# Performance work log

Hardware: AMD Instinct MI355X
Metric: run time of the kernel (lower is better)

The kernel has to match this reference:

```python
import jax, jax.numpy as jnp
import numpy as np

K_NEIGHBORS = 3
CLASSES = 5


def _l2_norm(x):
    # x: (N, C, H, W) -> (N, H*W, C), unit L2 norm over channel dim
    N, C, H, W = x.shape
    x = x.reshape(N, C, H * W).transpose(0, 2, 1)
    return x / jnp.linalg.norm(x, axis=-1, keepdims=True)


def setup_inputs() -> dict:
    key = jax.random.key(0)
    k1, k2 = jax.random.split(key)
    anchor = jax.random.normal(k1, (32, 64, 21, 21), dtype=jnp.float32)
    support_set = jax.random.normal(k2, (25, 64, 21, 21), dtype=jnp.float32)
    return {"anchor": anchor, "support_set": support_set, "av_num": 1, "sav_num": 1}


def reference(anchor, support_set, av_num, sav_num):
    # anchor: (B*AV, C, H, W), support_set: (L*S, C, H, W)
    q = _l2_norm(anchor)            # (B, HW, C)
    s = _l2_norm(support_set)       # (L*S, HW, C)
    C = s.shape[-1]
    s_flat = s.reshape(-1, C)       # (M, C), M = L*S*HW (class-major)
    # dense cosine similarity: (B, HW, M)
    sim = jnp.einsum('bqc,mc->bqm', q, s_flat)
    B, HW, M = sim.shape
    per_cls = M // CLASSES
    # (B//av, av, HW, L, S*HW)
    sim = sim.reshape(B // av_num, av_num, HW, CLASSES, per_cls)
    sim = jax.nn.sigmoid(sim)
    # av_num == 1 -> squeeze AV dim (matches torch squeeze(1) path)
    sim = sim[:, 0] if av_num == 1 else jnp.power(jnp.prod(sim, axis=1), 1.0 / av_num)
    # per-class top-k over descriptors, sum over k and over query locations
    topk = jax.lax.top_k(sim, K_NEIGHBORS)[0]        # (B, HW, L, K)
    i2c_sim = topk.sum(axis=-1).sum(axis=-2)         # (B, L)
    return i2c_sim
```

## Files before the change

### kernel.cpp

```cpp
#include <hip/hip_runtime.h>
#include <hip/hip_bf16.h>
#include <math.h>

#define CLASSES     5
#define C_DIM       64
#define HW          441
#define B_ANCH      32
#define NSUP        25
#define NROWS       (B_ANCH*HW)
#define MSUP        (NSUP*HW)
#define PER_CLS     (MSUP/CLASSES)
#define TILE_COLS   32
#define ROW_BYTES   (C_DIM*2)
#define TILE_BYTES  (TILE_COLS*ROW_BYTES)
#define PER_CLS_PAD 2304
#define NPAD        (PER_CLS_PAD - PER_CLS)
#define QUARTERS    4
#define TILES_PER_Q 18
#define ROWS_PER_BLK 128
#define NBLK_X      ((NROWS + ROWS_PER_BLK - 1) / ROWS_PER_BLK)

#define NEG_INF  (-1e30f)

typedef __bf16 bf16x8 __attribute__((ext_vector_type(8)));
typedef float  f32x4  __attribute__((ext_vector_type(4)));

#define TOP3_INS(v, t0, t1, t2) do {                              \
    float _v = (v);                                               \
    float _n0 = fmaxf(_v, (t0));                                  \
    float _n1 = __builtin_amdgcn_fmed3f(_v, (t0), (t1));          \
    float _n2 = __builtin_amdgcn_fmed3f(_v, (t1), (t2));          \
    (t0) = _n0; (t1) = _n1; (t2) = _n2; } while (0)

#define TRIPLE_MERGE(u0, u1, u2, v0, v1, v2) do {                 \
    float _A = fminf((u0), (v0));                                 \
    float _B = fmaxf((u1), (v1));                                 \
    float _E = fmaxf((u2), (v2));                                 \
    float _m0 = fmaxf((u0), (v0));                                \
    float _m1 = __builtin_amdgcn_fmed3f((u0), (v0), _B);          \
    float _m2 = __builtin_amdgcn_fmed3f(_A, _B, _E);              \
    (u0) = _m0; (u1) = _m1; (u2) = _m2; } while (0)

typedef __attribute__((address_space(1))) const void g_void;
typedef __attribute__((address_space(3))) void l_void;
__device__ __forceinline__ void gload_lds16(const void* g, void* l) {
    __builtin_amdgcn_global_load_lds((g_void*)g, (l_void*)l, 16, 0, 0);
}

#define MFMA16(A, B, C) __builtin_amdgcn_mfma_f32_16x16x32_bf16((A), (B), (C), 0, 0, 0)

__global__ __launch_bounds__(256) void norm_rows_kernel(
    const float* __restrict__ anchor, const float* __restrict__ support,
    __bf16* __restrict__ qb, __bf16* __restrict__ sb) {
    int r = blockIdx.x * 256 + threadIdx.x;
    const int total_main = MSUP + NROWS;
    if (r >= total_main) {
        int i = r - total_main;
        if (i < CLASSES * NPAD) {
            int cls = i / NPAD, ix = PER_CLS + i % NPAD;
            __bf16* op = sb + ((size_t)cls * PER_CLS_PAD + ix) * C_DIM;
            bf16x8 z = {};
            #pragma unroll
            for (int c0 = 0; c0 < C_DIM; c0 += 8) *(bf16x8*)(op + c0) = z;
        }
        return;
    }
    bool isSup = r < MSUP;
    int rc = isSup ? r : r - MSUP;
    const float* in = isSup ? support : anchor;
    int img = rc / HW, p = rc % HW;
    const float* base = in + (size_t)img * C_DIM * HW + p;
    float q[C_DIM];
    float ss = 0.f;
    #pragma unroll
    for (int c = 0; c < C_DIM; ++c) { q[c] = base[c * HW]; ss += q[c] * q[c]; }
    float sc = rsqrtf(ss);
    __bf16* op;
    if (isSup) {
        int cls = rc / PER_CLS, ix = rc - cls * PER_CLS;
        op = sb + ((size_t)cls * PER_CLS_PAD + ix) * C_DIM;
    } else {
        op = qb + (size_t)rc * C_DIM;
    }
    #pragma unroll
    for (int c0 = 0; c0 < C_DIM; c0 += 8) {
        bf16x8 v;
        #pragma unroll
        for (int j = 0; j < 8; ++j) v[j] = (__bf16)(q[c0 + j] * sc);
        *(bf16x8*)(op + c0) = v;
    }
}

template<int QNT, bool TAIL>
__device__ __forceinline__ void gemm_quarter(
    const char* stage_src,
    char* smem_base,
    const char* pB,
    int xoff0, int xoff1,
    int stage_dst_off,
    int lane, int lr,
    const bf16x8 a0[2], const bf16x8 a1[2],
    float t0[2][4], float t1[2][4], float t2[2][4]) {

    auto stage = [&](int buf, int tt) {
        gload_lds16(stage_src + tt * TILE_BYTES,
                    smem_base + buf * 4096 + stage_dst_off);
    };
    const f32x4 z = {0.f, 0.f, 0.f, 0.f};

    stage(0, 0);
    stage(1, 1);
    #pragma unroll
    for (int tt = 0; tt < QNT; ++tt) {
        if (tt < QNT - 1) asm volatile("s_waitcnt vmcnt(1)" ::: "memory");
        else              asm volatile("s_waitcnt vmcnt(0)" ::: "memory");
        __builtin_amdgcn_s_barrier();
        if (tt + 2 < QNT) stage((tt + 2) % 3, tt + 2);
        const int buf = tt % 3;
        const bool tail = TAIL && (tt == QNT - 1);
        const char* pb = pB + buf * 4096;
        bf16x8 b0 = *(const bf16x8*)(pb + xoff0);
        bf16x8 b1 = *(const bf16x8*)(pb + xoff1);
        bf16x8 b2 = *(const bf16x8*)(pb + 2048 + xoff0);
        bf16x8 b3 = *(const bf16x8*)(pb + 2048 + xoff1);
        f32x4 acc0, acc1, acc2, acc3;
        __builtin_amdgcn_s_setprio(1);
        acc0 = MFMA16(a0[0], b0, z); acc0 = MFMA16(a1[0], b1, acc0);
        acc1 = MFMA16(a0[1], b0, z); acc1 = MFMA16(a1[1], b1, acc1);
        acc2 = MFMA16(a0[0], b2, z); acc2 = MFMA16(a1[0], b3, acc2);
        acc3 = MFMA16(a0[1], b2, z); acc3 = MFMA16(a1[1], b3, acc3);
        __builtin_amdgcn_s_setprio(0);
        if (!tail) {
            #pragma unroll
            for (int j = 0; j < 4; ++j) {
                TOP3_INS(acc0[j], t0[0][j], t1[0][j], t2[0][j]);
                TOP3_INS(acc1[j], t0[1][j], t1[1][j], t2[1][j]);
                TOP3_INS(acc2[j], t0[0][j], t1[0][j], t2[0][j]);
                TOP3_INS(acc3[j], t0[1][j], t1[1][j], t2[1][j]);
            }
        } else {
            bool valid = lr < 13;
            #pragma unroll
            for (int j = 0; j < 4; ++j) {
                TOP3_INS(acc0[j], t0[0][j], t1[0][j], t2[0][j]);
                TOP3_INS(acc1[j], t0[1][j], t1[1][j], t2[1][j]);
                float v2 = valid ? acc2[j] : NEG_INF;
                float v3 = valid ? acc3[j] : NEG_INF;
                TOP3_INS(v2, t0[0][j], t1[0][j], t2[0][j]);
                TOP3_INS(v3, t0[1][j], t1[1][j], t2[1][j]);
            }
        }
    }
}

__global__ __launch_bounds__(256, 4) void knn_mfma_kernel(
    const __bf16* __restrict__ qb, const __bf16* __restrict__ sb,
    float* __restrict__ part) {
    __shared__ char smem[3][4096];

    int lane = threadIdx.x & 63;
    int w    = threadIdx.x >> 6;
    int lr   = lane & 15;
    int kg   = lane >> 4;
    int cls  = blockIdx.y >> 2;
    int q    = blockIdx.y & 3;
    int rowbase = blockIdx.x * ROWS_PER_BLK + w * 32;

    bf16x8 a0[2], a1[2];
    #pragma unroll
    for (int r = 0; r < 2; ++r) {
        int arow = rowbase + r * 16 + lr;
        int arc  = arow < NROWS ? arow : NROWS - 1;
        const bf16x8* qrow = (const bf16x8*)(qb + (size_t)arc * C_DIM);
        a0[r] = qrow[kg];
        a1[r] = qrow[4 + kg];
    }

    float t0[2][4], t1[2][4], t2[2][4];
    #pragma unroll
    for (int r = 0; r < 2; ++r)
        #pragma unroll
        for (int j = 0; j < 4; ++j) {
            t0[r][j] = NEG_INF; t1[r][j] = NEG_INF; t2[r][j] = NEG_INF;
        }

    int srow = lane >> 3;
    int sgrn = (lane & 7) ^ (srow & 7);
    int srcSwz = srow * 128 + sgrn * 16;
    const char* qbase = (const char*)sb
        + (size_t)cls * PER_CLS_PAD * ROW_BYTES
        + (size_t)q * TILES_PER_Q * TILE_BYTES;
    const char* stage_src = qbase + w * 1024 + srcSwz;
    int xoff0 = (((lr & 7) ^ kg) << 4);
    int xoff1 = xoff0 ^ 0x40;
    const char* pB = (const char*)smem + lr * 128;

    if (q == 3)
        gemm_quarter<15, true >(stage_src, (char*)smem, pB, xoff0, xoff1,
                                w * 1024, lane, lr, a0, a1, t0, t1, t2);
    else
        gemm_quarter<18, false>(stage_src, (char*)smem, pB, xoff0, xoff1,
                                w * 1024, lane, lr, a0, a1, t0, t1, t2);

    #pragma unroll
    for (int r = 0; r < 2; ++r) {
        #pragma unroll
        for (int j = 0; j < 4; ++j) {
            float u0 = t0[r][j], u1 = t1[r][j], u2 = t2[r][j];
            #pragma unroll
            for (int off = 1; off < 16; off <<= 1) {
                float v0 = __shfl_xor(u0, off, 64);
                float v1 = __shfl_xor(u1, off, 64);
                float v2 = __shfl_xor(u2, off, 64);
                TRIPLE_MERGE(u0, u1, u2, v0, v1, v2);
            }
            int row = rowbase + r * 16 + kg * 4 + j;
            if (lr == 0 && row < NROWS) {
                float* pp = part +
                    ((size_t)(row * CLASSES + cls) * QUARTERS + q) * 3;
                pp[0] = u0; pp[1] = u1; pp[2] = u2;
            }
        }
    }
}

__global__ __launch_bounds__(64) void merge_reduce_kernel(
    const float* __restrict__ part, float* __restrict__ out) {
    int bl = blockIdx.x;
    int b = bl / CLASSES;
    int l = bl % CLASSES;
    int lane = threadIdx.x;
    float acc = 0.f;
    for (int p = lane; p < HW; p += 64) {
        int row = b * HW + p;
        const float* pp = part + (size_t)(row * CLASSES + l) * (QUARTERS * 3);
        float u0 = pp[0], u1 = pp[1], u2 = pp[2];
        TRIPLE_MERGE(u0, u1, u2, pp[3], pp[4],  pp[5]);
        TRIPLE_MERGE(u0, u1, u2, pp[6], pp[7],  pp[8]);
        TRIPLE_MERGE(u0, u1, u2, pp[9], pp[10], pp[11]);
        acc += 1.f / (1.f + __expf(-u0))
             + 1.f / (1.f + __expf(-u1))
             + 1.f / (1.f + __expf(-u2));
    }
    #pragma unroll
    for (int off = 32; off; off >>= 1) acc += __shfl_xor(acc, off, 64);
    if (lane == 0) out[bl] = acc;
}

extern "C" void kernel_launch(void* const* d_in, const int* in_sizes, int n_in,
                              void* d_out, int out_size, void* d_ws, size_t ws_size,
                              hipStream_t stream) {
    const float* anchor  = (const float*)d_in[0];
    const float* support = (const float*)d_in[1];

    __bf16* sb = (__bf16*)d_ws;
    __bf16* qb = sb + (size_t)CLASSES * PER_CLS_PAD * C_DIM;
    float* part = (float*)(qb + (size_t)NROWS * C_DIM);

    {
        int total = MSUP + NROWS + CLASSES * NPAD;
        dim3 g((total + 255) / 256);
        norm_rows_kernel<<<g, 256, 0, stream>>>(anchor, support, qb, sb);
    }
    {
        dim3 g(NBLK_X, CLASSES * QUARTERS);
        knn_mfma_kernel<<<g, 256, 0, stream>>>(qb, sb, part);
    }
    {
        dim3 gm(B_ANCH * CLASSES);
        merge_reduce_kernel<<<gm, 64, 0, stream>>>(part, (float*)d_out);
    }
}
```

Before: 53.62 us.

## Double rows per wave to reuse each staged B tile across four A fragments

Each wave now handles 64 query rows (4 MFMA row fragments) instead of 32, so every support tile staged into LDS is reused against twice as many queries and half as many blocks restage the same support data. The MFMA issue is split into two half-tiles, with top-3 insertion of the first half interleaved with the LDS reads and MFMAs of the second. Register pressure roughly doubles for the top-3 state and A fragments, so the occupancy hint drops from 4 to 3 blocks per CU. Halving the grid also lowers the number of blocks available to fill the GPU.

```diff
diff --git a/kernel.cpp b/kernel.cpp
--- a/kernel.cpp
+++ b/kernel.cpp
@@ -17,7 +17,7 @@
 #define NPAD        (PER_CLS_PAD - PER_CLS)
 #define QUARTERS    4
 #define TILES_PER_Q 18
-#define ROWS_PER_BLK 128
+#define ROWS_PER_BLK 256
 #define NBLK_X      ((NROWS + ROWS_PER_BLK - 1) / ROWS_PER_BLK)
 
 #define NEG_INF  (-1e30f)
@@ -46,7 +46,6 @@
 __device__ __forceinline__ void gload_lds16(const void* g, void* l) {
     __builtin_amdgcn_global_load_lds((g_void*)g, (l_void*)l, 16, 0, 0);
 }
-
 #define MFMA16(A, B, C) __builtin_amdgcn_mfma_f32_16x16x32_bf16((A), (B), (C), 0, 0, 0)
 
 __global__ __launch_bounds__(256) void norm_rows_kernel(
@@ -93,21 +92,16 @@
 
 template<int QNT, bool TAIL>
 __device__ __forceinline__ void gemm_quarter(
-    const char* stage_src,
-    char* smem_base,
-    const char* pB,
-    int xoff0, int xoff1,
-    int stage_dst_off,
-    int lane, int lr,
-    const bf16x8 a0[2], const bf16x8 a1[2],
-    float t0[2][4], float t1[2][4], float t2[2][4]) {
+    const char* stage_src, char* smem_base, const char* pB,
+    int xoff0, int xoff1, int stage_dst_off, int lane, int lr,
+    const bf16x8 a0[4], const bf16x8 a1[4],
+    float t0[4][4], float t1[4][4], float t2[4][4]) {
 
     auto stage = [&](int buf, int tt) {
         gload_lds16(stage_src + tt * TILE_BYTES,
                     smem_base + buf * 4096 + stage_dst_off);
     };
     const f32x4 z = {0.f, 0.f, 0.f, 0.f};
-
     stage(0, 0);
     stage(1, 1);
     #pragma unroll
@@ -119,41 +113,53 @@
         const int buf = tt % 3;
         const bool tail = TAIL && (tt == QNT - 1);
         const char* pb = pB + buf * 4096;
+
         bf16x8 b0 = *(const bf16x8*)(pb + xoff0);
         bf16x8 b1 = *(const bf16x8*)(pb + xoff1);
+        f32x4 acc[4];
+        __builtin_amdgcn_s_setprio(1);
+        #pragma unroll
+        for (int r = 0; r < 4; ++r) {
+            acc[r] = MFMA16(a0[r], b0, z);
+            acc[r] = MFMA16(a1[r], b1, acc[r]);
+        }
+        __builtin_amdgcn_s_setprio(0);
         bf16x8 b2 = *(const bf16x8*)(pb + 2048 + xoff0);
         bf16x8 b3 = *(const bf16x8*)(pb + 2048 + xoff1);
-        f32x4 acc0, acc1, acc2, acc3;
+        #pragma unroll
+        for (int r = 0; r < 4; ++r)
+            #pragma unroll
+            for (int j = 0; j < 4; ++j)
+                TOP3_INS(acc[r][j], t0[r][j], t1[r][j], t2[r][j]);
+
+        f32x4 acd[4];
         __builtin_amdgcn_s_setprio(1);
-        acc0 = MFMA16(a0[0], b0, z); acc0 = MFMA16(a1[0], b1, acc0);
-        acc1 = MFMA16(a0[1], b0, z); acc1 = MFMA16(a1[1], b1, acc1);
-        acc2 = MFMA16(a0[0], b2, z); acc2 = MFMA16(a1[0], b3, acc2);
-        acc3 = MFMA16(a0[1], b2, z); acc3 = MFMA16(a1[1], b3, acc3);
+        #pragma unroll
+        for (int r = 0; r < 4; ++r) {
+            acd[r] = MFMA16(a0[r], b2, z);
+            acd[r] = MFMA16(a1[r], b3, acd[r]);
+        }
         __builtin_amdgcn_s_setprio(0);
         if (!tail) {
             #pragma unroll
-            for (int j = 0; j < 4; ++j) {
-                TOP3_INS(acc0[j], t0[0][j], t1[0][j], t2[0][j]);
-                TOP3_INS(acc1[j], t0[1][j], t1[1][j], t2[1][j]);
-                TOP3_INS(acc2[j], t0[0][j], t1[0][j], t2[0][j]);
-                TOP3_INS(acc3[j], t0[1][j], t1[1][j], t2[1][j]);
-            }
+            for (int r = 0; r < 4; ++r)
+                #pragma unroll
+                for (int j = 0; j < 4; ++j)
+                    TOP3_INS(acd[r][j], t0[r][j], t1[r][j], t2[r][j]);
         } else {
             bool valid = lr < 13;
             #pragma unroll
-            for (int j = 0; j < 4; ++j) {
-                TOP3_INS(acc0[j], t0[0][j], t1[0][j], t2[0][j]);
-                TOP3_INS(acc1[j], t0[1][j], t1[1][j], t2[1][j]);
-                float v2 = valid ? acc2[j] : NEG_INF;
-                float v3 = valid ? acc3[j] : NEG_INF;
-                TOP3_INS(v2, t0[0][j], t1[0][j], t2[0][j]);
-                TOP3_INS(v3, t0[1][j], t1[1][j], t2[1][j]);
-            }
-        }
-    }
-}
-
-__global__ __launch_bounds__(256, 4) void knn_mfma_kernel(
+            for (int r = 0; r < 4; ++r)
+                #pragma unroll
+                for (int j = 0; j < 4; ++j) {
+                    float v = valid ? acd[r][j] : NEG_INF;
+                    TOP3_INS(v, t0[r][j], t1[r][j], t2[r][j]);
+                }
+        }
+    }
+}
+
+__global__ __launch_bounds__(256, 3) void knn_mfma_kernel(
     const __bf16* __restrict__ qb, const __bf16* __restrict__ sb,
     float* __restrict__ part) {
     __shared__ char smem[3][4096];
@@ -164,11 +170,11 @@
     int kg   = lane >> 4;
     int cls  = blockIdx.y >> 2;
     int q    = blockIdx.y & 3;
-    int rowbase = blockIdx.x * ROWS_PER_BLK + w * 32;
-
-    bf16x8 a0[2], a1[2];
-    #pragma unroll
-    for (int r = 0; r < 2; ++r) {
+    int rowbase = blockIdx.x * ROWS_PER_BLK + w * 64;
+
+    bf16x8 a0[4], a1[4];
+    #pragma unroll
+    for (int r = 0; r < 4; ++r) {
         int arow = rowbase + r * 16 + lr;
         int arc  = arow < NROWS ? arow : NROWS - 1;
         const bf16x8* qrow = (const bf16x8*)(qb + (size_t)arc * C_DIM);
@@ -176,9 +182,9 @@
         a1[r] = qrow[4 + kg];
     }
 
-    float t0[2][4], t1[2][4], t2[2][4];
-    #pragma unroll
-    for (int r = 0; r < 2; ++r)
+    float t0[4][4], t1[4][4], t2[4][4];
+    #pragma unroll
+    for (int r = 0; r < 4; ++r)
         #pragma unroll
         for (int j = 0; j < 4; ++j) {
             t0[r][j] = NEG_INF; t1[r][j] = NEG_INF; t2[r][j] = NEG_INF;
@@ -203,7 +209,7 @@
                                 w * 1024, lane, lr, a0, a1, t0, t1, t2);
 
     #pragma unroll
-    for (int r = 0; r < 2; ++r) {
+    for (int r = 0; r < 4; ++r) {
         #pragma unroll
         for (int j = 0; j < 4; ++j) {
             float u0 = t0[r][j], u1 = t1[r][j], u2 = t2[r][j];
```

New measurement: 56.77 us. 5.9% more time.

## Prefetch next LDS tile into registers and deepen staging ring to four buffers

Applied to the files above, without the earlier changes.

The kernel now reads the next tile's B fragments from LDS into a second register set before running the MFMAs on the current tile. It also grows the async global-to-LDS staging from three to four buffers, issuing loads three tiles ahead. The aim is to hide LDS read latency behind MFMA and top-3 work and to keep loads further ahead. In exchange it uses more registers for the extra fragments and 4 KB more shared memory per block, which may reduce occupancy under launch_bounds(256,4).

```diff
diff --git a/kernel.cpp b/kernel.cpp
--- a/kernel.cpp
+++ b/kernel.cpp
@@ -46,7 +46,6 @@
 __device__ __forceinline__ void gload_lds16(const void* g, void* l) {
     __builtin_amdgcn_global_load_lds((g_void*)g, (l_void*)l, 16, 0, 0);
 }
-
 #define MFMA16(A, B, C) __builtin_amdgcn_mfma_f32_16x16x32_bf16((A), (B), (C), 0, 0, 0)
 
 __global__ __launch_bounds__(256) void norm_rows_kernel(
@@ -93,12 +92,8 @@
 
 template<int QNT, bool TAIL>
 __device__ __forceinline__ void gemm_quarter(
-    const char* stage_src,
-    char* smem_base,
-    const char* pB,
-    int xoff0, int xoff1,
-    int stage_dst_off,
-    int lane, int lr,
+    const char* stage_src, char* smem_base, const char* pB,
+    int xoff0, int xoff1, int stage_dst_off, int lane, int lr,
     const bf16x8 a0[2], const bf16x8 a1[2],
     float t0[2][4], float t1[2][4], float t2[2][4]) {
 
@@ -106,30 +101,46 @@
         gload_lds16(stage_src + tt * TILE_BYTES,
                     smem_base + buf * 4096 + stage_dst_off);
     };
+    auto ldsread = [&](int buf, bf16x8 b[4]) {
+        const char* pb = pB + buf * 4096;
+        b[0] = *(const bf16x8*)(pb + xoff0);
+        b[1] = *(const bf16x8*)(pb + xoff1);
+        b[2] = *(const bf16x8*)(pb + 2048 + xoff0);
+        b[3] = *(const bf16x8*)(pb + 2048 + xoff1);
+    };
     const f32x4 z = {0.f, 0.f, 0.f, 0.f};
 
     stage(0, 0);
     stage(1, 1);
-    #pragma unroll
-    for (int tt = 0; tt < QNT; ++tt) {
-        if (tt < QNT - 1) asm volatile("s_waitcnt vmcnt(1)" ::: "memory");
-        else              asm volatile("s_waitcnt vmcnt(0)" ::: "memory");
-        __builtin_amdgcn_s_barrier();
-        if (tt + 2 < QNT) stage((tt + 2) % 3, tt + 2);
-        const int buf = tt % 3;
-        const bool tail = TAIL && (tt == QNT - 1);
-        const char* pb = pB + buf * 4096;
-        bf16x8 b0 = *(const bf16x8*)(pb + xoff0);
-        bf16x8 b1 = *(const bf16x8*)(pb + xoff1);
-        bf16x8 b2 = *(const bf16x8*)(pb + 2048 + xoff0);
-        bf16x8 b3 = *(const bf16x8*)(pb + 2048 + xoff1);
+    asm volatile("s_waitcnt vmcnt(1)" ::: "memory");
+    __builtin_amdgcn_s_barrier();
+    bf16x8 bA[4], bB[4];
+    ldsread(0, bA);
+    stage(2, 2);
+
+    #pragma unroll
+    for (int t = 0; t < QNT; ++t) {
+        if (t < QNT - 1) {
+            if (t <= QNT - 3) asm volatile("s_waitcnt vmcnt(1)" ::: "memory");
+            else              asm volatile("s_waitcnt vmcnt(0)" ::: "memory");
+            __builtin_amdgcn_s_barrier();
+        }
+        if (t < QNT - 1) {
+            if (t & 1) ldsread((t + 1) % 4, bA);
+            else       ldsread((t + 1) % 4, bB);
+        }
+        if (t + 3 < QNT) stage((t + 3) % 4, t + 3);
+
+        const bf16x8* bc = (t & 1) ? bB : bA;
         f32x4 acc0, acc1, acc2, acc3;
         __builtin_amdgcn_s_setprio(1);
-        acc0 = MFMA16(a0[0], b0, z); acc0 = MFMA16(a1[0], b1, acc0);
-        acc1 = MFMA16(a0[1], b0, z); acc1 = MFMA16(a1[1], b1, acc1);
-        acc2 = MFMA16(a0[0], b2, z); acc2 = MFMA16(a1[0], b3, acc2);
-        acc3 = MFMA16(a0[1], b2, z); acc3 = MFMA16(a1[1], b3, acc3);
+        acc0 = MFMA16(a0[0], bc[0], z); acc0 = MFMA16(a1[0], bc[1], acc0);
+        acc1 = MFMA16(a0[1], bc[0], z); acc1 = MFMA16(a1[1], bc[1], acc1);
+        acc2 = MFMA16(a0[0], bc[2], z); acc2 = MFMA16(a1[0], bc[3], acc2);
+        acc3 = MFMA16(a0[1], bc[2], z); acc3 = MFMA16(a1[1], bc[3], acc3);
         __builtin_amdgcn_s_setprio(0);
+
+        const bool tail = TAIL && (t == QNT - 1);
         if (!tail) {
             #pragma unroll
             for (int j = 0; j < 4; ++j) {
@@ -156,7 +167,7 @@
 __global__ __launch_bounds__(256, 4) void knn_mfma_kernel(
     const __bf16* __restrict__ qb, const __bf16* __restrict__ sb,
     float* __restrict__ part) {
-    __shared__ char smem[3][4096];
+    __shared__ char smem[4][4096];
 
     int lane = threadIdx.x & 63;
     int w    = threadIdx.x >> 6;
```

Measured after the change: 53.52 us. No clear change (-0.2%).
